# Kernel optimization log

Hardware: AMD Instinct MI355X
Metric: run time of the kernel (lower is better)

Reference implementation:

```python
import jax, jax.numpy as jnp
import numpy as np

R, S, V, F = 4096, 128, 3, 35  # n_rays, n_samples, n_views(=3 fixed by rgb_fc), in_feat_ch+3


def _kaiming(key, fan_out, fan_in):
    return jax.random.normal(key, (fan_out, fan_in), jnp.float32) * jnp.sqrt(2.0 / fan_in)


def setup_inputs() -> dict:
    key = jax.random.key(0)
    ks = jax.random.split(key, 8)
    rgb_feat = jax.random.normal(ks[0], (R, S, V, F), jnp.float32)
    # base_fc: 105 -> 64 -> 32
    bw1, bw2 = _kaiming(ks[1], 64, 105), _kaiming(ks[2], 32, 64)
    # vis_fc: 32 -> 32 -> 32
    vw1, vw2 = _kaiming(ks[3], 32, 32), _kaiming(ks[4], 32, 32)
    # rgb_fc: 96 -> 32 -> 16 -> 3
    rw1, rw2, rw3 = _kaiming(ks[5], 32, 96), _kaiming(ks[6], 16, 32), _kaiming(ks[7], 3, 16)
    z = jnp.zeros
    return {
        "rgb_feat": rgb_feat,
        "bw1": bw1, "bb1": z((64,)), "bw2": bw2, "bb2": z((32,)),
        "vw1": vw1, "vb1": z((32,)), "vw2": vw2, "vb2": z((32,)),
        "rw1": rw1, "rb1": z((32,)), "rw2": rw2, "rb2": z((16,)), "rw3": rw3, "rb3": z((3,)),
    }


def _lin(x, w, b):
    return x @ w.T + b


def reference(rgb_feat, bw1, bb1, bw2, bb2, vw1, vb1, vw2, vb2,
              rw1, rb1, rw2, rb2, rw3, rb3):
    elu = jax.nn.elu
    num_views = rgb_feat.shape[2]
    rgb_in = rgb_feat[..., :3]
    # fused mean/variance over the views axis (dim=2)
    mean = jnp.mean(rgb_feat, axis=2, keepdims=True)          # [R,S,1,F]
    var = jnp.mean((rgb_feat - mean) ** 2, axis=2, keepdims=True)
    globalfeat = jnp.concatenate([mean, var], axis=-1)         # [R,S,1,2F]
    x = jnp.concatenate(
        [jnp.broadcast_to(globalfeat, (rgb_feat.shape[0], rgb_feat.shape[1], num_views, globalfeat.shape[-1])),
         rgb_feat], axis=-1)                                   # [R,S,V,3F]
    x = elu(_lin(elu(_lin(x, bw1, bb1)), bw2, bb2))            # [R,S,V,32]
    x_vis = elu(_lin(elu(_lin(x / num_views, vw1, vb1)), vw2, vb2))
    x = x + x_vis
    h = x.reshape(x.shape[0], x.shape[1], num_views * 32)      # [R,S,96]
    rgb_out = jax.nn.sigmoid(_lin(elu(_lin(elu(_lin(h, rw1, rb1)), rw2, rb2)), rw3, rb3))
    return (rgb_in, rgb_out)
```

## Files before the change

### kernel.cpp

```cpp
#include <hip/hip_runtime.h>
#include <hip/hip_bf16.h>

#define NPTS      524288
#define OUT2_BASE 4718592
#define NBLK32    16384

using bf16x8 = __attribute__((ext_vector_type(8))) short;
using f32x4  = __attribute__((ext_vector_type(4))) float;


__device__ __forceinline__ ushort f2bf(float f) {
    union { float f; unsigned u; } v; v.f = f;
    unsigned u = v.u;
    unsigned r = u + 0x7fffu + ((u >> 16) & 1u);
    return (ushort)(r >> 16);
}
__device__ __forceinline__ uint pack2(float a, float b) {
    union { __hip_bfloat162 h; uint u; } cv;
    cv.h = __float22bfloat162_rn(make_float2(a, b));
    return cv.u;
}
__device__ __forceinline__ float eluf(float x) {
    return fmaxf(x, 0.f) + __expf(fminf(x, 0.f)) - 1.f;
}
__device__ __forceinline__ float sigm(float x) { return 1.f / (1.f + __expf(-x)); }

__device__ __forceinline__ void load8(const float* __restrict__ p, float* d) {
    __builtin_memcpy(d, p, 16);
    __builtin_memcpy(d + 4, p + 4, 16);
}

__global__ void prep_k(const float* __restrict__ bw1, const float* __restrict__ bw2,
                       const float* __restrict__ vw1, const float* __restrict__ vw2,
                       const float* __restrict__ rw1, const float* __restrict__ rw2,
                       ushort* __restrict__ w)
{
    int i = blockIdx.x * 256 + threadIdx.x;
    if (i < 6144) {
        int n = i / 96, k = i % 96;
        float val = 0.f;
        if (k < 35)                 val = bw1[n * 105 + k];
        else if (k >= 40 && k < 75) val = bw1[n * 105 + 35 + (k - 40)];
        w[i] = f2bf(val);
    } else if (i < 10752) {
        int t = i - 6144, n = t / 72, k = t % 72;
        w[i] = f2bf(k < 35 ? bw1[n * 105 + 70 + k] : 0.f);
    } else if (i < 13056) {
        int t = i - 10752, n = t / 72, k = t % 72;
        w[i] = f2bf(k < 64 ? bw2[n * 64 + k] : 0.f);
    } else if (i < 14336) {
        int t = i - 13056, n = t / 40, k = t % 40;
        w[i] = f2bf(k < 32 ? vw1[n * 32 + k] * (1.f / 3.f) : 0.f);
    } else if (i < 15616) {
        int t = i - 14336, n = t / 40, k = t % 40;
        w[i] = f2bf(k < 32 ? vw2[n * 32 + k] : 0.f);
    } else if (i < 18944) {
        int t = i - 15616, n = t / 104, k = t % 104;
        w[i] = f2bf(k < 96 ? rw1[n * 96 + k] : 0.f);
    } else if (i < 19584) {
        int t = i - 18944, n = t / 40, k = t % 40;
        w[i] = f2bf(k < 32 ? rw2[n * 32 + k] : 0.f);
    }
}

__global__ __launch_bounds__(256, 4) void mlp_k(
    const float* __restrict__ feat, const ushort* __restrict__ w,
    const float* __restrict__ bb1, const float* __restrict__ bb2,
    const float* __restrict__ vb1, const float* __restrict__ vb2,
    const float* __restrict__ rb1, const float* __restrict__ rb2,
    const float* __restrict__ rw3, const float* __restrict__ rb3,
    float* __restrict__ out)
{
    __shared__ __align__(16) ushort shA[6912];
    __shared__ __align__(16) ushort shB[3328];
    __shared__ __align__(16) ushort shC[6912];

    const int tid  = threadIdx.x;
    const int wave = tid >> 6;
    const int wv2  = wave >> 1;
    const int wvn  = wave & 1;
    const int lane = tid & 63;
    const int n16  = lane & 15;
    const int quad = lane >> 4;
    const int prow = wv2 * 16 + n16;
    const long long pbase = (long long)blockIdx.x * 32;

    const ushort* WG = w;
    const ushort* WF = w + 6144;
    const ushort* W2 = w + 10752;
    const ushort* V1 = w + 13056;
    const ushort* V2 = w + 14336;
    const ushort* R1 = w + 15616;
    const ushort* R2 = w + 18944;

    const float4 bb1q0 = *(const float4*)(bb1 + (wvn * 2 + 0) * 16 + quad * 4);
    const float4 bb1q1 = *(const float4*)(bb1 + (wvn * 2 + 1) * 16 + quad * 4);
    const float4 bb2q  = *(const float4*)(bb2 + wvn * 16 + quad * 4);
    const float4 vb1q  = *(const float4*)(vb1 + wvn * 16 + quad * 4);
    const float4 vb2q  = *(const float4*)(vb2 + wvn * 16 + quad * 4);
    const float4 rb1q  = *(const float4*)(rb1 + wvn * 16 + quad * 4);
    const float4 rb2q  = *(const float4*)(rb2 + quad * 4);

    {
        const uint4 z = make_uint4(0u, 0u, 0u, 0u);
        uint4* zc = (uint4*)shC;
        for (int i = tid; i < 288; i += 256) {
            int r = i / 3, c = i - r * 3;
            zc[r * 9 + 5 + c] = z;
        }
        if (tid < 64) {
            uint4* zb = (uint4*)shB;
            int r = tid >> 1, c = tid & 1;
            zb[r * 12 + 10 + c] = z;
        }
        float* o1 = out + pbase * 9;
        for (int i = tid; i < 288; i += 256) {
            int p = i / 9, r = i - p * 9, v = r / 3, c = r - v * 3;
            o1[i] = feat[(pbase + p) * 105 + v * 35 + c];
        }
        if (tid < 160) {
            int p  = tid / 5;
            int g  = tid - p * 5;
            int k8 = g * 8;
            const float* row = feat + (pbase + p) * 105;
            float X0[8], X1[8], X2[8];
            load8(row + k8,      X0);
            load8(row + 35 + k8, X1);
            if (k8 == 32 && (pbase + p) == (long long)NPTS - 1) {
                X2[0] = row[102]; X2[1] = row[103]; X2[2] = row[104];
                X2[3] = 0.f; X2[4] = 0.f; X2[5] = 0.f; X2[6] = 0.f; X2[7] = 0.f;
            } else {
                load8(row + 70 + k8, X2);
            }
            float M[8], VV[8];
#pragma unroll
            for (int j = 0; j < 8; ++j) {
                float a = X0[j], b = X1[j], c = X2[j];
                float m  = (a + b + c) * (1.f / 3.f);
                float da = a - m, db = b - m, dc = c - m;
                M[j]  = m;
                VV[j] = (da * da + db * db + dc * dc) * (1.f / 3.f);
            }
            *(uint4*)(shC + p * 72 + k8) =
                make_uint4(pack2(X0[0], X0[1]), pack2(X0[2], X0[3]),
                           pack2(X0[4], X0[5]), pack2(X0[6], X0[7]));
            *(uint4*)(shC + (32 + p) * 72 + k8) =
                make_uint4(pack2(X1[0], X1[1]), pack2(X1[2], X1[3]),
                           pack2(X1[4], X1[5]), pack2(X1[6], X1[7]));
            *(uint4*)(shC + (64 + p) * 72 + k8) =
                make_uint4(pack2(X2[0], X2[1]), pack2(X2[2], X2[3]),
                           pack2(X2[4], X2[5]), pack2(X2[6], X2[7]));
            *(uint4*)(shB + p * 96 + k8) =
                make_uint4(pack2(M[0], M[1]), pack2(M[2], M[3]),
                           pack2(M[4], M[5]), pack2(M[6], M[7]));
            *(uint4*)(shB + p * 96 + 40 + k8) =
                make_uint4(pack2(VV[0], VV[1]), pack2(VV[2], VV[3]),
                           pack2(VV[4], VV[5]), pack2(VV[6], VV[7]));
        }
    }
    __syncthreads();

    const f32x4 Z = {0.f, 0.f, 0.f, 0.f};

    f32x4 Cg[2]    = {Z, Z};
    f32x4 Cf[3][2] = {{Z, Z}, {Z, Z}, {Z, Z}};
#pragma unroll
    for (int ks = 0; ks < 3; ++ks) {
        bf16x8 xg = *(const bf16x8*)(shB + prow * 96 + ks * 32 + quad * 8);
#pragma unroll
        for (int ntl = 0; ntl < 2; ++ntl) {
            bf16x8 wg = *(const bf16x8*)(WG + ((wvn * 2 + ntl) * 16 + n16) * 96 + ks * 32 + quad * 8);
            Cg[ntl] = __builtin_amdgcn_mfma_f32_16x16x32_bf16(wg, xg, Cg[ntl], 0, 0, 0);
        }
    }
#pragma unroll
    for (int ks = 0; ks < 2; ++ks) {
        bf16x8 x0 = *(const bf16x8*)(shC + (0 * 32 + prow) * 72 + ks * 32 + quad * 8);
        bf16x8 x1 = *(const bf16x8*)(shC + (1 * 32 + prow) * 72 + ks * 32 + quad * 8);
        bf16x8 x2 = *(const bf16x8*)(shC + (2 * 32 + prow) * 72 + ks * 32 + quad * 8);
#pragma unroll
        for (int ntl = 0; ntl < 2; ++ntl) {
            bf16x8 wf = *(const bf16x8*)(WF + ((wvn * 2 + ntl) * 16 + n16) * 72 + ks * 32 + quad * 8);
            Cf[0][ntl] = __builtin_amdgcn_mfma_f32_16x16x32_bf16(wf, x0, Cf[0][ntl], 0, 0, 0);
            Cf[1][ntl] = __builtin_amdgcn_mfma_f32_16x16x32_bf16(wf, x1, Cf[1][ntl], 0, 0, 0);
            Cf[2][ntl] = __builtin_amdgcn_mfma_f32_16x16x32_bf16(wf, x2, Cf[2][ntl], 0, 0, 0);
        }
    }
#pragma unroll
    for (int mt = 0; mt < 3; ++mt)
#pragma unroll
        for (int ntl = 0; ntl < 2; ++ntl) {
            const float4 bq = ntl ? bb1q1 : bb1q0;
            float e0 = eluf(Cf[mt][ntl][0] + Cg[ntl][0] + bq.x);
            float e1 = eluf(Cf[mt][ntl][1] + Cg[ntl][1] + bq.y);
            float e2 = eluf(Cf[mt][ntl][2] + Cg[ntl][2] + bq.z);
            float e3 = eluf(Cf[mt][ntl][3] + Cg[ntl][3] + bq.w);
            uint2 u; u.x = pack2(e0, e1); u.y = pack2(e2, e3);
            *(uint2*)(shA + (mt * 32 + prow) * 72 + (wvn * 2 + ntl) * 16 + quad * 4) = u;
        }
    __syncthreads();

    f32x4 C2[3] = {Z, Z, Z};
#pragma unroll
    for (int ks = 0; ks < 2; ++ks) {
        bf16x8 x0 = *(const bf16x8*)(shA + (0 * 32 + prow) * 72 + ks * 32 + quad * 8);
        bf16x8 x1 = *(const bf16x8*)(shA + (1 * 32 + prow) * 72 + ks * 32 + quad * 8);
        bf16x8 x2 = *(const bf16x8*)(shA + (2 * 32 + prow) * 72 + ks * 32 + quad * 8);
        bf16x8 w2 = *(const bf16x8*)(W2 + (wvn * 16 + n16) * 72 + ks * 32 + quad * 8);
        C2[0] = __builtin_amdgcn_mfma_f32_16x16x32_bf16(w2, x0, C2[0], 0, 0, 0);
        C2[1] = __builtin_amdgcn_mfma_f32_16x16x32_bf16(w2, x1, C2[1], 0, 0, 0);
        C2[2] = __builtin_amdgcn_mfma_f32_16x16x32_bf16(w2, x2, C2[2], 0, 0, 0);
    }
    float h2r[3][4];
#pragma unroll
    for (int mt = 0; mt < 3; ++mt) {
        float e0 = eluf(C2[mt][0] + bb2q.x);
        float e1 = eluf(C2[mt][1] + bb2q.y);
        float e2 = eluf(C2[mt][2] + bb2q.z);
        float e3 = eluf(C2[mt][3] + bb2q.w);
        h2r[mt][0] = e0; h2r[mt][1] = e1; h2r[mt][2] = e2; h2r[mt][3] = e3;
        uint2 u; u.x = pack2(e0, e1); u.y = pack2(e2, e3);
        *(uint2*)(shC + (mt * 32 + prow) * 72 + wvn * 16 + quad * 4) = u;
    }
    __syncthreads();

    f32x4 T1[3] = {Z, Z, Z};
    {
        bf16x8 x0 = *(const bf16x8*)(shC + (0 * 32 + prow) * 72 + quad * 8);
        bf16x8 x1 = *(const bf16x8*)(shC + (1 * 32 + prow) * 72 + quad * 8);
        bf16x8 x2 = *(const bf16x8*)(shC + (2 * 32 + prow) * 72 + quad * 8);
        bf16x8 v1 = *(const bf16x8*)(V1 + (wvn * 16 + n16) * 40 + quad * 8);
        T1[0] = __builtin_amdgcn_mfma_f32_16x16x32_bf16(v1, x0, T1[0], 0, 0, 0);
        T1[1] = __builtin_amdgcn_mfma_f32_16x16x32_bf16(v1, x1, T1[1], 0, 0, 0);
        T1[2] = __builtin_amdgcn_mfma_f32_16x16x32_bf16(v1, x2, T1[2], 0, 0, 0);
    }
#pragma unroll
    for (int mt = 0; mt < 3; ++mt) {
        float e0 = eluf(T1[mt][0] + vb1q.x);
        float e1 = eluf(T1[mt][1] + vb1q.y);
        float e2 = eluf(T1[mt][2] + vb1q.z);
        float e3 = eluf(T1[mt][3] + vb1q.w);
        uint2 u; u.x = pack2(e0, e1); u.y = pack2(e2, e3);
        *(uint2*)(shA + (mt * 32 + prow) * 72 + wvn * 16 + quad * 4) = u;
    }
    __syncthreads();

    f32x4 T2[3] = {Z, Z, Z};
    {
        bf16x8 x0 = *(const bf16x8*)(shA + (0 * 32 + prow) * 72 + quad * 8);
        bf16x8 x1 = *(const bf16x8*)(shA + (1 * 32 + prow) * 72 + quad * 8);
        bf16x8 x2 = *(const bf16x8*)(shA + (2 * 32 + prow) * 72 + quad * 8);
        bf16x8 v2 = *(const bf16x8*)(V2 + (wvn * 16 + n16) * 40 + quad * 8);
        T2[0] = __builtin_amdgcn_mfma_f32_16x16x32_bf16(v2, x0, T2[0], 0, 0, 0);
        T2[1] = __builtin_amdgcn_mfma_f32_16x16x32_bf16(v2, x1, T2[1], 0, 0, 0);
        T2[2] = __builtin_amdgcn_mfma_f32_16x16x32_bf16(v2, x2, T2[2], 0, 0, 0);
    }
#pragma unroll
    for (int mt = 0; mt < 3; ++mt) {
        float x0 = h2r[mt][0] + eluf(T2[mt][0] + vb2q.x);
        float x1 = h2r[mt][1] + eluf(T2[mt][1] + vb2q.y);
        float x2v = h2r[mt][2] + eluf(T2[mt][2] + vb2q.z);
        float x3 = h2r[mt][3] + eluf(T2[mt][3] + vb2q.w);
        uint2 u; u.x = pack2(x0, x1); u.y = pack2(x2v, x3);
        *(uint2*)(shB + prow * 104 + mt * 32 + wvn * 16 + quad * 4) = u;
    }
    __syncthreads();

    f32x4 CR = Z;
#pragma unroll
    for (int ks = 0; ks < 3; ++ks) {
        bf16x8 xb = *(const bf16x8*)(shB + prow * 104 + ks * 32 + quad * 8);
        bf16x8 r1w = *(const bf16x8*)(R1 + (wvn * 16 + n16) * 104 + ks * 32 + quad * 8);
        CR = __builtin_amdgcn_mfma_f32_16x16x32_bf16(r1w, xb, CR, 0, 0, 0);
    }
    {
        float e0 = eluf(CR[0] + rb1q.x);
        float e1 = eluf(CR[1] + rb1q.y);
        float e2 = eluf(CR[2] + rb1q.z);
        float e3 = eluf(CR[3] + rb1q.w);
        uint2 u; u.x = pack2(e0, e1); u.y = pack2(e2, e3);
        *(uint2*)(shC + prow * 40 + wvn * 16 + quad * 4) = u;
    }
    __syncthreads();

    f32x4 C3 = Z;
    {
        bf16x8 xb = *(const bf16x8*)(shC + prow * 40 + quad * 8);
        bf16x8 r2w = *(const bf16x8*)(R2 + n16 * 40 + quad * 8);
        C3 = __builtin_amdgcn_mfma_f32_16x16x32_bf16(r2w, xb, C3, 0, 0, 0);
    }
    if (wvn == 0) {
        float4 rv;
        rv.x = eluf(C3[0] + rb2q.x);
        rv.y = eluf(C3[1] + rb2q.y);
        rv.z = eluf(C3[2] + rb2q.z);
        rv.w = eluf(C3[3] + rb2q.w);
        *(float4*)((float*)shA + prow * 20 + quad * 4) = rv;
    }
    __syncthreads();

    if (tid < 96) {
        const float* r2b = (const float*)shA;
        int p = tid / 3, c = tid - p * 3;
        const float4* rr = (const float4*)(r2b + p * 20);
        const float4* w3 = (const float4*)(rw3 + c * 16);
        float4 a0 = rr[0], a1 = rr[1], a2 = rr[2], a3 = rr[3];
        float4 q0 = w3[0], q1 = w3[1], q2 = w3[2], q3 = w3[3];
        float s = rb3[c];
        s += a0.x * q0.x + a0.y * q0.y + a0.z * q0.z + a0.w * q0.w;
        s += a1.x * q1.x + a1.y * q1.y + a1.z * q1.z + a1.w * q1.w;
        s += a2.x * q2.x + a2.y * q2.y + a2.z * q2.z + a2.w * q2.w;
        s += a3.x * q3.x + a3.y * q3.y + a3.z * q3.z + a3.w * q3.w;
        out[OUT2_BASE + pbase * 3 + tid] = sigm(s);
    }
}

extern "C" void kernel_launch(void* const* d_in, const int* in_sizes, int n_in,
                              void* d_out, int out_size, void* d_ws, size_t ws_size,
                              hipStream_t stream) {
    const float* feat = (const float*)d_in[0];
    const float* bw1  = (const float*)d_in[1];
    const float* bb1  = (const float*)d_in[2];
    const float* bw2  = (const float*)d_in[3];
    const float* bb2  = (const float*)d_in[4];
    const float* vw1  = (const float*)d_in[5];
    const float* vb1  = (const float*)d_in[6];
    const float* vw2  = (const float*)d_in[7];
    const float* vb2  = (const float*)d_in[8];
    const float* rw1  = (const float*)d_in[9];
    const float* rb1  = (const float*)d_in[10];
    const float* rw2  = (const float*)d_in[11];
    const float* rb2  = (const float*)d_in[12];
    const float* rw3  = (const float*)d_in[13];
    const float* rb3  = (const float*)d_in[14];
    ushort* w  = (ushort*)d_ws;
    float* out = (float*)d_out;

    hipLaunchKernelGGL(prep_k, dim3(77), dim3(256), 0, stream,
                       bw1, bw2, vw1, vw2, rw1, rw2, w);
    hipLaunchKernelGGL(mlp_k, dim3(NBLK32), dim3(256), 0, stream,
                       feat, w, bb1, bb2, vb1, vb2, rb1, rb2, rw3, rb3, out);
}
```

Before: 422.0 us.

## Make each wave own 16 points end-to-end, drop block barriers

Restructures the MLP kernel so each wave processes its own 16 points through all layers. The block now covers 64 points instead of 32, and waves no longer split output columns. Inputs are loaded straight into registers in MFMA operand layout, with the mean/variance operands assembled by ds_bpermute instead of going through shared memory. Each wave gets a private, XOR-swizzled LDS region, so all __syncthreads are removed and the final 16->3 layer is done with lane shuffles. The aim is to cut barrier stalls and LDS traffic, at the cost of more registers per wave and redundant weight loads per wave.

```diff
diff --git a/kernel.cpp b/kernel.cpp
--- a/kernel.cpp
+++ b/kernel.cpp
@@ -3,10 +3,12 @@
 
 #define NPTS      524288
 #define OUT2_BASE 4718592
-#define NBLK32    16384
+#define NBLK64    8192
 
 using bf16x8 = __attribute__((ext_vector_type(8))) short;
 using f32x4  = __attribute__((ext_vector_type(4))) float;
+
+#define MFMA(a, b, c) __builtin_amdgcn_mfma_f32_16x16x32_bf16(a, b, c, 0, 0, 0)
 
 
 __device__ __forceinline__ ushort f2bf(float f) {
@@ -29,6 +31,18 @@
     __builtin_memcpy(d, p, 16);
     __builtin_memcpy(d + 4, p + 4, 16);
 }
+__device__ __forceinline__ bf16x8 pk8(const float* x) {
+    union { uint4 u; bf16x8 h; } cv;
+    cv.u = make_uint4(pack2(x[0], x[1]), pack2(x[2], x[3]),
+                      pack2(x[4], x[5]), pack2(x[6], x[7]));
+    return cv.h;
+}
+__device__ __forceinline__ bf16x8 pk4u(uint a, uint b, uint c, uint d) {
+    union { uint4 u; bf16x8 h; } cv;
+    cv.u = make_uint4(a, b, c, d);
+    return cv.h;
+}
+__device__ __forceinline__ bf16x8 ldw(const ushort* p) { return *(const bf16x8*)p; }
 
 __global__ void prep_k(const float* __restrict__ bw1, const float* __restrict__ bw2,
                        const float* __restrict__ vw1, const float* __restrict__ vw2,
@@ -71,19 +85,21 @@
     const float* __restrict__ rw3, const float* __restrict__ rb3,
     float* __restrict__ out)
 {
-    __shared__ __align__(16) ushort shA[6912];
-    __shared__ __align__(16) ushort shB[3328];
-    __shared__ __align__(16) ushort shC[6912];
+    __shared__ __align__(16) ushort sh[4][4608];
 
     const int tid  = threadIdx.x;
     const int wave = tid >> 6;
-    const int wv2  = wave >> 1;
-    const int wvn  = wave & 1;
     const int lane = tid & 63;
     const int n16  = lane & 15;
     const int quad = lane >> 4;
-    const int prow = wv2 * 16 + n16;
-    const long long pbase = (long long)blockIdx.x * 32;
+    char* const RA = (char*)sh[wave];
+    char* const RB = (char*)sh[wave] + 6144;
+    const int sw7 = n16 & 7;
+    const int sw3 = n16 & 3;
+
+    const long long pbase = (long long)blockIdx.x * 64 + wave * 16;
+    const long long pt    = pbase + n16;
+    const float* row = feat + pt * 105;
 
     const ushort* WG = w;
     const ushort* WF = w + 6144;
@@ -93,225 +109,184 @@
     const ushort* R1 = w + 15616;
     const ushort* R2 = w + 18944;
 
-    const float4 bb1q0 = *(const float4*)(bb1 + (wvn * 2 + 0) * 16 + quad * 4);
-    const float4 bb1q1 = *(const float4*)(bb1 + (wvn * 2 + 1) * 16 + quad * 4);
-    const float4 bb2q  = *(const float4*)(bb2 + wvn * 16 + quad * 4);
-    const float4 vb1q  = *(const float4*)(vb1 + wvn * 16 + quad * 4);
-    const float4 vb2q  = *(const float4*)(vb2 + wvn * 16 + quad * 4);
-    const float4 rb1q  = *(const float4*)(rb1 + wvn * 16 + quad * 4);
-    const float4 rb2q  = *(const float4*)(rb2 + quad * 4);
-
     {
-        const uint4 z = make_uint4(0u, 0u, 0u, 0u);
-        uint4* zc = (uint4*)shC;
-        for (int i = tid; i < 288; i += 256) {
-            int r = i / 3, c = i - r * 3;
-            zc[r * 9 + 5 + c] = z;
-        }
-        if (tid < 64) {
-            uint4* zb = (uint4*)shB;
-            int r = tid >> 1, c = tid & 1;
-            zb[r * 12 + 10 + c] = z;
-        }
         float* o1 = out + pbase * 9;
-        for (int i = tid; i < 288; i += 256) {
-            int p = i / 9, r = i - p * 9, v = r / 3, c = r - v * 3;
-            o1[i] = feat[(pbase + p) * 105 + v * 35 + c];
-        }
-        if (tid < 160) {
-            int p  = tid / 5;
-            int g  = tid - p * 5;
-            int k8 = g * 8;
-            const float* row = feat + (pbase + p) * 105;
-            float X0[8], X1[8], X2[8];
-            load8(row + k8,      X0);
-            load8(row + 35 + k8, X1);
-            if (k8 == 32 && (pbase + p) == (long long)NPTS - 1) {
-                X2[0] = row[102]; X2[1] = row[103]; X2[2] = row[104];
-                X2[3] = 0.f; X2[4] = 0.f; X2[5] = 0.f; X2[6] = 0.f; X2[7] = 0.f;
-            } else {
-                load8(row + 70 + k8, X2);
+        const float* f0 = feat + pbase * 105;
+#pragma unroll
+        for (int t = 0; t < 3; ++t) {
+            int i = lane + t * 64;
+            if (t < 2 || lane < 16) {
+                int p = i / 9, r = i - p * 9, v = r / 3, c = r - v * 3;
+                o1[i] = f0[p * 105 + v * 35 + c];
             }
-            float M[8], VV[8];
-#pragma unroll
-            for (int j = 0; j < 8; ++j) {
-                float a = X0[j], b = X1[j], c = X2[j];
-                float m  = (a + b + c) * (1.f / 3.f);
-                float da = a - m, db = b - m, dc = c - m;
-                M[j]  = m;
-                VV[j] = (da * da + db * db + dc * dc) * (1.f / 3.f);
-            }
-            *(uint4*)(shC + p * 72 + k8) =
-                make_uint4(pack2(X0[0], X0[1]), pack2(X0[2], X0[3]),
-                           pack2(X0[4], X0[5]), pack2(X0[6], X0[7]));
-            *(uint4*)(shC + (32 + p) * 72 + k8) =
-                make_uint4(pack2(X1[0], X1[1]), pack2(X1[2], X1[3]),
-                           pack2(X1[4], X1[5]), pack2(X1[6], X1[7]));
-            *(uint4*)(shC + (64 + p) * 72 + k8) =
-                make_uint4(pack2(X2[0], X2[1]), pack2(X2[2], X2[3]),
-                           pack2(X2[4], X2[5]), pack2(X2[6], X2[7]));
-            *(uint4*)(shB + p * 96 + k8) =
-                make_uint4(pack2(M[0], M[1]), pack2(M[2], M[3]),
-                           pack2(M[4], M[5]), pack2(M[6], M[7]));
-            *(uint4*)(shB + p * 96 + 40 + k8) =
-                make_uint4(pack2(VV[0], VV[1]), pack2(VV[2], VV[3]),
-                           pack2(VV[4], VV[5]), pack2(VV[6], VV[7]));
-        }
-    }
-    __syncthreads();
+        }
+    }
+
+    float A0[8], A1[8], A2[8];
+    load8(row + 8 * quad,      A0);
+    load8(row + 35 + 8 * quad, A1);
+    load8(row + 70 + 8 * quad, A2);
+    float E0[8] = {0,0,0,0,0,0,0,0}, E1[8] = {0,0,0,0,0,0,0,0}, E2[8] = {0,0,0,0,0,0,0,0};
+    if (quad == 0) {
+        load8(row + 32, E0);
+        load8(row + 67, E1);
+        if (pt == (long long)NPTS - 1) {
+            E2[0] = row[102]; E2[1] = row[103]; E2[2] = row[104];
+        } else {
+            load8(row + 102, E2);
+        }
+    }
+    float M[8], Vv[8], M4[8], V4[8];
+#pragma unroll
+    for (int j = 0; j < 8; ++j) {
+        float a = A0[j], b = A1[j], c = A2[j];
+        float m = (a + b + c) * (1.f / 3.f);
+        float da = a - m, db = b - m, dc = c - m;
+        M[j] = m; Vv[j] = (da * da + db * db + dc * dc) * (1.f / 3.f);
+        float a4 = E0[j], b4 = E1[j], c4 = E2[j];
+        float m4 = (a4 + b4 + c4) * (1.f / 3.f);
+        float e4 = a4 - m4, f4 = b4 - m4, g4 = c4 - m4;
+        M4[j] = m4; V4[j] = (e4 * e4 + f4 * f4 + g4 * g4) * (1.f / 3.f);
+    }
+    uint vPK[4], v4PK[4], m4PK[4];
+#pragma unroll
+    for (int i = 0; i < 4; ++i) {
+        vPK[i]  = pack2(Vv[2 * i], Vv[2 * i + 1]);
+        v4PK[i] = pack2(V4[2 * i], V4[2 * i + 1]);
+        m4PK[i] = pack2(M4[2 * i], M4[2 * i + 1]);
+    }
+    bf16x8 XAv[3], XBv[3];
+    XAv[0] = pk8(A0); XAv[1] = pk8(A1); XAv[2] = pk8(A2);
+    const bf16x8 ZF = pk4u(0u, 0u, 0u, 0u);
+    XBv[0] = ZF; XBv[1] = ZF; XBv[2] = ZF;
+    if (quad == 0) { XBv[0] = pk8(E0); XBv[1] = pk8(E1); XBv[2] = pk8(E2); }
+    const bf16x8 G0 = pk8(M);
+    const int prevAddr = ((lane + 48) & 63) * 4;
+    uint G1u[4], G2u[4];
+#pragma unroll
+    for (int i = 0; i < 4; ++i) {
+        uint bv  = (uint)__builtin_amdgcn_ds_bpermute(prevAddr, (int)vPK[i]);
+        uint bv4 = (uint)__builtin_amdgcn_ds_bpermute(prevAddr, (int)v4PK[i]);
+        G1u[i] = (quad == 0) ? m4PK[i] : bv;
+        G2u[i] = (quad == 0) ? bv : ((quad == 1) ? bv4 : 0u);
+    }
+    const bf16x8 G1 = pk4u(G1u[0], G1u[1], G1u[2], G1u[3]);
+    const bf16x8 G2 = pk4u(G2u[0], G2u[1], G2u[2], G2u[3]);
 
     const f32x4 Z = {0.f, 0.f, 0.f, 0.f};
 
-    f32x4 Cg[2]    = {Z, Z};
-    f32x4 Cf[3][2] = {{Z, Z}, {Z, Z}, {Z, Z}};
-#pragma unroll
-    for (int ks = 0; ks < 3; ++ks) {
-        bf16x8 xg = *(const bf16x8*)(shB + prow * 96 + ks * 32 + quad * 8);
-#pragma unroll
-        for (int ntl = 0; ntl < 2; ++ntl) {
-            bf16x8 wg = *(const bf16x8*)(WG + ((wvn * 2 + ntl) * 16 + n16) * 96 + ks * 32 + quad * 8);
-            Cg[ntl] = __builtin_amdgcn_mfma_f32_16x16x32_bf16(wg, xg, Cg[ntl], 0, 0, 0);
-        }
-    }
-#pragma unroll
-    for (int ks = 0; ks < 2; ++ks) {
-        bf16x8 x0 = *(const bf16x8*)(shC + (0 * 32 + prow) * 72 + ks * 32 + quad * 8);
-        bf16x8 x1 = *(const bf16x8*)(shC + (1 * 32 + prow) * 72 + ks * 32 + quad * 8);
-        bf16x8 x2 = *(const bf16x8*)(shC + (2 * 32 + prow) * 72 + ks * 32 + quad * 8);
-#pragma unroll
-        for (int ntl = 0; ntl < 2; ++ntl) {
-            bf16x8 wf = *(const bf16x8*)(WF + ((wvn * 2 + ntl) * 16 + n16) * 72 + ks * 32 + quad * 8);
-            Cf[0][ntl] = __builtin_amdgcn_mfma_f32_16x16x32_bf16(wf, x0, Cf[0][ntl], 0, 0, 0);
-            Cf[1][ntl] = __builtin_amdgcn_mfma_f32_16x16x32_bf16(wf, x1, Cf[1][ntl], 0, 0, 0);
-            Cf[2][ntl] = __builtin_amdgcn_mfma_f32_16x16x32_bf16(wf, x2, Cf[2][ntl], 0, 0, 0);
-        }
-    }
-#pragma unroll
-    for (int mt = 0; mt < 3; ++mt)
-#pragma unroll
-        for (int ntl = 0; ntl < 2; ++ntl) {
-            const float4 bq = ntl ? bb1q1 : bb1q0;
-            float e0 = eluf(Cf[mt][ntl][0] + Cg[ntl][0] + bq.x);
-            float e1 = eluf(Cf[mt][ntl][1] + Cg[ntl][1] + bq.y);
-            float e2 = eluf(Cf[mt][ntl][2] + Cg[ntl][2] + bq.z);
-            float e3 = eluf(Cf[mt][ntl][3] + Cg[ntl][3] + bq.w);
+#pragma unroll
+    for (int ntl = 0; ntl < 4; ++ntl) {
+        const ushort* WGb = WG + (ntl * 16 + n16) * 96 + quad * 8;
+        f32x4 Cg = MFMA(ldw(WGb), G0, Z);
+        Cg = MFMA(ldw(WGb + 32), G1, Cg);
+        Cg = MFMA(ldw(WGb + 64), G2, Cg);
+        const ushort* WFb = WF + (ntl * 16 + n16) * 72 + quad * 8;
+        const bf16x8 wf0 = ldw(WFb), wf1 = ldw(WFb + 32);
+        const float4 bq = *(const float4*)(bb1 + ntl * 16 + quad * 4);
+#pragma unroll
+        for (int v = 0; v < 3; ++v) {
+            f32x4 C = MFMA(wf0, XAv[v], Cg);
+            C = MFMA(wf1, XBv[v], C);
+            float e0 = eluf(C[0] + bq.x), e1 = eluf(C[1] + bq.y);
+            float e2 = eluf(C[2] + bq.z), e3 = eluf(C[3] + bq.w);
             uint2 u; u.x = pack2(e0, e1); u.y = pack2(e2, e3);
-            *(uint2*)(shA + (mt * 32 + prow) * 72 + (wvn * 2 + ntl) * 16 + quad * 4) = u;
-        }
-    __syncthreads();
-
-    f32x4 C2[3] = {Z, Z, Z};
-#pragma unroll
-    for (int ks = 0; ks < 2; ++ks) {
-        bf16x8 x0 = *(const bf16x8*)(shA + (0 * 32 + prow) * 72 + ks * 32 + quad * 8);
-        bf16x8 x1 = *(const bf16x8*)(shA + (1 * 32 + prow) * 72 + ks * 32 + quad * 8);
-        bf16x8 x2 = *(const bf16x8*)(shA + (2 * 32 + prow) * 72 + ks * 32 + quad * 8);
-        bf16x8 w2 = *(const bf16x8*)(W2 + (wvn * 16 + n16) * 72 + ks * 32 + quad * 8);
-        C2[0] = __builtin_amdgcn_mfma_f32_16x16x32_bf16(w2, x0, C2[0], 0, 0, 0);
-        C2[1] = __builtin_amdgcn_mfma_f32_16x16x32_bf16(w2, x1, C2[1], 0, 0, 0);
-        C2[2] = __builtin_amdgcn_mfma_f32_16x16x32_bf16(w2, x2, C2[2], 0, 0, 0);
-    }
-    float h2r[3][4];
-#pragma unroll
-    for (int mt = 0; mt < 3; ++mt) {
-        float e0 = eluf(C2[mt][0] + bb2q.x);
-        float e1 = eluf(C2[mt][1] + bb2q.y);
-        float e2 = eluf(C2[mt][2] + bb2q.z);
-        float e3 = eluf(C2[mt][3] + bb2q.w);
-        h2r[mt][0] = e0; h2r[mt][1] = e1; h2r[mt][2] = e2; h2r[mt][3] = e3;
+            int slot = (ntl * 2 + (quad >> 1)) ^ sw7;
+            *(uint2*)(RA + v * 2048 + n16 * 128 + slot * 16 + (quad & 1) * 8) = u;
+        }
+    }
+
+    float h2r[3][2][4];
+#pragma unroll
+    for (int v = 0; v < 3; ++v) {
+        const bf16x8 ha = *(const bf16x8*)(RA + v * 2048 + n16 * 128 + ((0 + quad) ^ sw7) * 16);
+        const bf16x8 hb = *(const bf16x8*)(RA + v * 2048 + n16 * 128 + ((4 + quad) ^ sw7) * 16);
+#pragma unroll
+        for (int n2 = 0; n2 < 2; ++n2) {
+            const ushort* W2b = W2 + (n2 * 16 + n16) * 72 + quad * 8;
+            f32x4 C = MFMA(ldw(W2b), ha, Z);
+            C = MFMA(ldw(W2b + 32), hb, C);
+            const float4 bq = *(const float4*)(bb2 + n2 * 16 + quad * 4);
+            float e0 = eluf(C[0] + bq.x), e1 = eluf(C[1] + bq.y);
+            float e2 = eluf(C[2] + bq.z), e3 = eluf(C[3] + bq.w);
+            h2r[v][n2][0] = e0; h2r[v][n2][1] = e1;
+            h2r[v][n2][2] = e2; h2r[v][n2][3] = e3;
+            uint2 u; u.x = pack2(e0, e1); u.y = pack2(e2, e3);
+            int slot = (n2 * 2 + (quad >> 1)) ^ sw3;
+            *(uint2*)(RB + v * 1024 + n16 * 64 + slot * 16 + (quad & 1) * 8) = u;
+        }
+    }
+
+#pragma unroll
+    for (int v = 0; v < 3; ++v) {
+        const bf16x8 hf = *(const bf16x8*)(RB + v * 1024 + n16 * 64 + ((quad ^ sw3) * 16));
+#pragma unroll
+        for (int n2 = 0; n2 < 2; ++n2) {
+            f32x4 C = MFMA(ldw(V1 + (n2 * 16 + n16) * 40 + quad * 8), hf, Z);
+            const float4 bq = *(const float4*)(vb1 + n2 * 16 + quad * 4);
+            float e0 = eluf(C[0] + bq.x), e1 = eluf(C[1] + bq.y);
+            float e2 = eluf(C[2] + bq.z), e3 = eluf(C[3] + bq.w);
+            uint2 u; u.x = pack2(e0, e1); u.y = pack2(e2, e3);
+            int slot = (n2 * 2 + (quad >> 1)) ^ sw3;
+            *(uint2*)(RA + v * 1024 + n16 * 64 + slot * 16 + (quad & 1) * 8) = u;
+        }
+    }
+
+#pragma unroll
+    for (int v = 0; v < 3; ++v) {
+        const bf16x8 tf = *(const bf16x8*)(RA + v * 1024 + n16 * 64 + ((quad ^ sw3) * 16));
+#pragma unroll
+        for (int n2 = 0; n2 < 2; ++n2) {
+            f32x4 C = MFMA(ldw(V2 + (n2 * 16 + n16) * 40 + quad * 8), tf, Z);
+            const float4 bq = *(const float4*)(vb2 + n2 * 16 + quad * 4);
+            float x0 = h2r[v][n2][0] + eluf(C[0] + bq.x);
+            float x1 = h2r[v][n2][1] + eluf(C[1] + bq.y);
+            float x2v = h2r[v][n2][2] + eluf(C[2] + bq.z);
+            float x3 = h2r[v][n2][3] + eluf(C[3] + bq.w);
+            uint2 u; u.x = pack2(x0, x1); u.y = pack2(x2v, x3);
+            int slot = (4 * v + 2 * n2 + (quad >> 1)) ^ sw3;
+            *(uint2*)(RB + n16 * 192 + slot * 16 + (quad & 1) * 8) = u;
+        }
+    }
+
+    f32x4 CR[2] = {Z, Z};
+#pragma unroll
+    for (int v = 0; v < 3; ++v) {
+        const bf16x8 xf = *(const bf16x8*)(RB + n16 * 192 + (((4 * v + quad) ^ sw3) * 16));
+#pragma unroll
+        for (int n2 = 0; n2 < 2; ++n2)
+            CR[n2] = MFMA(ldw(R1 + (n2 * 16 + n16) * 104 + v * 32 + quad * 8), xf, CR[n2]);
+    }
+#pragma unroll
+    for (int n2 = 0; n2 < 2; ++n2) {
+        const float4 bq = *(const float4*)(rb1 + n2 * 16 + quad * 4);
+        float e0 = eluf(CR[n2][0] + bq.x), e1 = eluf(CR[n2][1] + bq.y);
+        float e2 = eluf(CR[n2][2] + bq.z), e3 = eluf(CR[n2][3] + bq.w);
         uint2 u; u.x = pack2(e0, e1); u.y = pack2(e2, e3);
-        *(uint2*)(shC + (mt * 32 + prow) * 72 + wvn * 16 + quad * 4) = u;
-    }
-    __syncthreads();
-
-    f32x4 T1[3] = {Z, Z, Z};
-    {
-        bf16x8 x0 = *(const bf16x8*)(shC + (0 * 32 + prow) * 72 + quad * 8);
-        bf16x8 x1 = *(const bf16x8*)(shC + (1 * 32 + prow) * 72 + quad * 8);
-        bf16x8 x2 = *(const bf16x8*)(shC + (2 * 32 + prow) * 72 + quad * 8);
-        bf16x8 v1 = *(const bf16x8*)(V1 + (wvn * 16 + n16) * 40 + quad * 8);
-        T1[0] = __builtin_amdgcn_mfma_f32_16x16x32_bf16(v1, x0, T1[0], 0, 0, 0);
-        T1[1] = __builtin_amdgcn_mfma_f32_16x16x32_bf16(v1, x1, T1[1], 0, 0, 0);
-        T1[2] = __builtin_amdgcn_mfma_f32_16x16x32_bf16(v1, x2, T1[2], 0, 0, 0);
-    }
-#pragma unroll
-    for (int mt = 0; mt < 3; ++mt) {
-        float e0 = eluf(T1[mt][0] + vb1q.x);
-        float e1 = eluf(T1[mt][1] + vb1q.y);
-        float e2 = eluf(T1[mt][2] + vb1q.z);
-        float e3 = eluf(T1[mt][3] + vb1q.w);
-        uint2 u; u.x = pack2(e0, e1); u.y = pack2(e2, e3);
-        *(uint2*)(shA + (mt * 32 + prow) * 72 + wvn * 16 + quad * 4) = u;
-    }
-    __syncthreads();
-
-    f32x4 T2[3] = {Z, Z, Z};
-    {
-        bf16x8 x0 = *(const bf16x8*)(shA + (0 * 32 + prow) * 72 + quad * 8);
-        bf16x8 x1 = *(const bf16x8*)(shA + (1 * 32 + prow) * 72 + quad * 8);
-        bf16x8 x2 = *(const bf16x8*)(shA + (2 * 32 + prow) * 72 + quad * 8);
-        bf16x8 v2 = *(const bf16x8*)(V2 + (wvn * 16 + n16) * 40 + quad * 8);
-        T2[0] = __builtin_amdgcn_mfma_f32_16x16x32_bf16(v2, x0, T2[0], 0, 0, 0);
-        T2[1] = __builtin_amdgcn_mfma_f32_16x16x32_bf16(v2, x1, T2[1], 0, 0, 0);
-        T2[2] = __builtin_amdgcn_mfma_f32_16x16x32_bf16(v2, x2, T2[2], 0, 0, 0);
-    }
-#pragma unroll
-    for (int mt = 0; mt < 3; ++mt) {
-        float x0 = h2r[mt][0] + eluf(T2[mt][0] + vb2q.x);
-        float x1 = h2r[mt][1] + eluf(T2[mt][1] + vb2q.y);
-        float x2v = h2r[mt][2] + eluf(T2[mt][2] + vb2q.z);
-        float x3 = h2r[mt][3] + eluf(T2[mt][3] + vb2q.w);
-        uint2 u; u.x = pack2(x0, x1); u.y = pack2(x2v, x3);
-        *(uint2*)(shB + prow * 104 + mt * 32 + wvn * 16 + quad * 4) = u;
-    }
-    __syncthreads();
-
-    f32x4 CR = Z;
-#pragma unroll
-    for (int ks = 0; ks < 3; ++ks) {
-        bf16x8 xb = *(const bf16x8*)(shB + prow * 104 + ks * 32 + quad * 8);
-        bf16x8 r1w = *(const bf16x8*)(R1 + (wvn * 16 + n16) * 104 + ks * 32 + quad * 8);
-        CR = __builtin_amdgcn_mfma_f32_16x16x32_bf16(r1w, xb, CR, 0, 0, 0);
-    }
-    {
-        float e0 = eluf(CR[0] + rb1q.x);
-        float e1 = eluf(CR[1] + rb1q.y);
-        float e2 = eluf(CR[2] + rb1q.z);
-        float e3 = eluf(CR[3] + rb1q.w);
-        uint2 u; u.x = pack2(e0, e1); u.y = pack2(e2, e3);
-        *(uint2*)(shC + prow * 40 + wvn * 16 + quad * 4) = u;
-    }
-    __syncthreads();
-
-    f32x4 C3 = Z;
-    {
-        bf16x8 xb = *(const bf16x8*)(shC + prow * 40 + quad * 8);
-        bf16x8 r2w = *(const bf16x8*)(R2 + n16 * 40 + quad * 8);
-        C3 = __builtin_amdgcn_mfma_f32_16x16x32_bf16(r2w, xb, C3, 0, 0, 0);
-    }
-    if (wvn == 0) {
-        float4 rv;
-        rv.x = eluf(C3[0] + rb2q.x);
-        rv.y = eluf(C3[1] + rb2q.y);
-        rv.z = eluf(C3[2] + rb2q.z);
-        rv.w = eluf(C3[3] + rb2q.w);
-        *(float4*)((float*)shA + prow * 20 + quad * 4) = rv;
-    }
-    __syncthreads();
-
-    if (tid < 96) {
-        const float* r2b = (const float*)shA;
-        int p = tid / 3, c = tid - p * 3;
-        const float4* rr = (const float4*)(r2b + p * 20);
-        const float4* w3 = (const float4*)(rw3 + c * 16);
-        float4 a0 = rr[0], a1 = rr[1], a2 = rr[2], a3 = rr[3];
-        float4 q0 = w3[0], q1 = w3[1], q2 = w3[2], q3 = w3[3];
-        float s = rb3[c];
-        s += a0.x * q0.x + a0.y * q0.y + a0.z * q0.z + a0.w * q0.w;
-        s += a1.x * q1.x + a1.y * q1.y + a1.z * q1.z + a1.w * q1.w;
-        s += a2.x * q2.x + a2.y * q2.y + a2.z * q2.z + a2.w * q2.w;
-        s += a3.x * q3.x + a3.y * q3.y + a3.z * q3.z + a3.w * q3.w;
-        out[OUT2_BASE + pbase * 3 + tid] = sigm(s);
+        int slot = (n2 * 2 + (quad >> 1)) ^ sw3;
+        *(uint2*)(RA + n16 * 64 + slot * 16 + (quad & 1) * 8) = u;
+    }
+
+    const bf16x8 rf = *(const bf16x8*)(RA + n16 * 64 + ((quad ^ sw3) * 16));
+    f32x4 C3 = MFMA(ldw(R2 + n16 * 40 + quad * 8), rf, Z);
+    const float4 bq2 = *(const float4*)(rb2 + quad * 4);
+    float r0 = eluf(C3[0] + bq2.x), r1v = eluf(C3[1] + bq2.y);
+    float r2v = eluf(C3[2] + bq2.z), r3 = eluf(C3[3] + bq2.w);
+
+    const float4 w30 = *(const float4*)(rw3 + 0 * 16 + quad * 4);
+    const float4 w31 = *(const float4*)(rw3 + 1 * 16 + quad * 4);
+    const float4 w32 = *(const float4*)(rw3 + 2 * 16 + quad * 4);
+    float s0 = r0 * w30.x + r1v * w30.y + r2v * w30.z + r3 * w30.w;
+    float s1 = r0 * w31.x + r1v * w31.y + r2v * w31.z + r3 * w31.w;
+    float s2 = r0 * w32.x + r1v * w32.y + r2v * w32.z + r3 * w32.w;
+    s0 += __shfl_xor(s0, 16); s0 += __shfl_xor(s0, 32);
+    s1 += __shfl_xor(s1, 16); s1 += __shfl_xor(s1, 32);
+    s2 += __shfl_xor(s2, 16); s2 += __shfl_xor(s2, 32);
+    if (quad == 0) {
+        float* o2 = out + OUT2_BASE + pt * 3;
+        o2[0] = sigm(s0 + rb3[0]);
+        o2[1] = sigm(s1 + rb3[1]);
+        o2[2] = sigm(s2 + rb3[2]);
     }
 }
 
@@ -338,6 +313,6 @@
 
     hipLaunchKernelGGL(prep_k, dim3(77), dim3(256), 0, stream,
                        bw1, bw2, vw1, vw2, rw1, rw2, w);
-    hipLaunchKernelGGL(mlp_k, dim3(NBLK32), dim3(256), 0, stream,
+    hipLaunchKernelGGL(mlp_k, dim3(NBLK64), dim3(256), 0, stream,
                        feat, w, bb1, bb2, vb1, vb2, rb1, rb2, rw3, rb3, out);
 }
```

After: 433.9 us. 2.8% more time.
